# Kernel optimization log

Hardware: AMD Instinct MI355X
Metric: run time of the kernel (lower is better)

Reference implementation:

```python
import jax, jax.numpy as jnp
import numpy as np

B, L1, CTX_TXT, C, NH, HD = 2, 4096, 512, 2048, 16, 128
IMG_LEN = 257           # hard-coded image-context length in WanI2VCrossAttentionProcessor
L2 = IMG_LEN + CTX_TXT
EPS = 1e-6


def setup_inputs() -> dict:
    key = jax.random.key(0)
    ks = jax.random.split(key, 16)
    s = 0.02
    w = lambda k: jax.random.normal(k, (C, C), jnp.float32) * s
    bvec = lambda k: jax.random.normal(k, (C,), jnp.float32) * s
    return {
        "x": jax.random.normal(ks[0], (B, L1, C), jnp.float32),
        "context": jax.random.normal(ks[1], (B, L2, C), jnp.float32),
        "context_lens": jax.random.randint(ks[2], (B,), 1, CTX_TXT + 1, jnp.int32),
        "Wq": w(ks[3]), "bq": bvec(ks[4]), "gq": jnp.ones((C,), jnp.float32),
        "Wk": w(ks[5]), "bk": bvec(ks[6]), "gk": jnp.ones((C,), jnp.float32),
        "Wv": w(ks[7]), "bv": bvec(ks[8]),
        "Wki": w(ks[9]), "bki": bvec(ks[10]), "gki": jnp.ones((C,), jnp.float32),
        "Wvi": w(ks[11]), "bvi": bvec(ks[12]),
        "Wo": w(ks[13]), "bo": bvec(ks[14]),
    }


def rms_norm(x, g):
    # RMSNorm over full channel dim (applied before head reshape, as in source)
    return x * jax.lax.rsqrt(jnp.mean(x * x, axis=-1, keepdims=True) + EPS) * g


def attention(q, k, v, key_mask=None):
    # q: [b, Lq, n, d]; k, v: [b, Lk, n, d]
    scale = 1.0 / np.sqrt(HD).astype(np.float32)
    scores = jnp.einsum('bqnd,bknd->bnqk', q, k) * scale
    if key_mask is not None:
        scores = jnp.where(key_mask, scores, jnp.finfo(scores.dtype).min)
    probs = jax.nn.softmax(scores, axis=-1)
    return jnp.einsum('bnqk,bknd->bqnd', probs, v)


def reference(x, context, context_lens, Wq, bq, gq, Wk, bk, gk, Wv, bv,
              Wki, bki, gki, Wvi, bvi, Wo, bo):
    b = x.shape[0]
    ctx_img = context[:, :IMG_LEN]
    ctx_txt = context[:, IMG_LEN:]

    q = rms_norm(x @ Wq + bq, gq).reshape(b, -1, NH, HD)
    k = rms_norm(ctx_txt @ Wk + bk, gk).reshape(b, -1, NH, HD)
    v = (ctx_txt @ Wv + bv).reshape(b, -1, NH, HD)
    k_img = rms_norm(ctx_img @ Wki + bki, gki).reshape(b, -1, NH, HD)
    v_img = (ctx_img @ Wvi + bvi).reshape(b, -1, NH, HD)

    img_x = attention(q, k_img, v_img)  # no k_lens on image branch
    key_mask = (jnp.arange(CTX_TXT)[None, :] < context_lens[:, None])[:, None, None, :]
    txt_x = attention(q, k, v, key_mask)

    out = (txt_x + img_x).reshape(b, -1, NH * HD)
    return out @ Wo + bo
```

## Files before the change

kernel.cpp:

```cpp
#include <hip/hip_runtime.h>

typedef unsigned short u16;
typedef short short8 __attribute__((ext_vector_type(8)));
typedef float f32x4 __attribute__((ext_vector_type(4)));
typedef unsigned short u16x4 __attribute__((ext_vector_type(4)));

__device__ __forceinline__ u16 f2bf(float f) {
  unsigned u = __builtin_bit_cast(unsigned, f);
  u += 0x7fffu + ((u >> 16) & 1u);
  return (u16)(u >> 16);
}
__device__ __forceinline__ float bf2f(u16 s) {
  unsigned u = ((unsigned)s) << 16;
  return __builtin_bit_cast(float, u);
}
__device__ __forceinline__ unsigned cvtpk_bf16(float a, float b) {
  unsigned r;
  asm("v_cvt_pk_bf16_f32 %0, %1, %2" : "=v"(r) : "v"(a), "v"(b));
  return r;
}

#if __has_builtin(__builtin_amdgcn_exp2f)
#define EXP2F(x) __builtin_amdgcn_exp2f(x)
#else
#define EXP2F(x) exp2f(x)
#endif

#define MFMA32(a, b, c) __builtin_amdgcn_mfma_f32_16x16x32_bf16(a, b, c, 0, 0, 0)

#define GLDS16(gp, lp)                                                         \
  __builtin_amdgcn_global_load_lds(                                            \
      (__attribute__((address_space(1))) void*)(gp),                           \
      (__attribute__((address_space(3))) void*)(lp), 16, 0, 0)

__global__ __launch_bounds__(256) void cast_bf16_k(const float* __restrict__ in,
                                                   u16* __restrict__ out, int n4) {
  int i = blockIdx.x * 256 + threadIdx.x;
  if (i >= n4) return;
  float4 v = ((const float4*)in)[i];
  u16x4 o = { f2bf(v.x), f2bf(v.y), f2bf(v.z), f2bf(v.w) };
  ((u16x4*)out)[i] = o;
}

__global__ __launch_bounds__(256) void transw_k(const float* W0, const float* W1,
                                                const float* W2, const float* W3,
                                                const float* W4, const float* W5,
                                                u16* __restrict__ Wt) {
  int z = blockIdx.z;
  const float* W = z == 0 ? W0 : z == 1 ? W1 : z == 2 ? W2 : z == 3 ? W3 : z == 4 ? W4 : W5;
  u16* T = Wt + (size_t)z * 2048 * 2048;
  __shared__ float tile[64][65];
  int k0 = blockIdx.x * 64, n0 = blockIdx.y * 64;
  int c4 = (threadIdx.x & 15) * 4;
  int r = threadIdx.x >> 4;
#pragma unroll
  for (int i = 0; i < 4; ++i) {
    int row = r + i * 16;
    float4 v = *(const float4*)(W + (size_t)(k0 + row) * 2048 + n0 + c4);
    tile[row][c4 + 0] = v.x; tile[row][c4 + 1] = v.y;
    tile[row][c4 + 2] = v.z; tile[row][c4 + 3] = v.w;
  }
  __syncthreads();
#pragma unroll
  for (int i = 0; i < 4; ++i) {
    int nrow = r + i * 16;
    u16x4 o = { f2bf(tile[c4 + 0][nrow]), f2bf(tile[c4 + 1][nrow]),
                f2bf(tile[c4 + 2][nrow]), f2bf(tile[c4 + 3][nrow]) };
    *(u16x4*)(T + (size_t)(n0 + nrow) * 2048 + k0 + c4) = o;
  }
}

struct GemmJob {
  const u16* A; const u16* Bt; const float* bias; void* out;
  int M; int mode; int ldo;
};
struct GemmJobs { GemmJob j[8]; };

__global__ __launch_bounds__(256) void gemm_k(GemmJobs jobs) {
  GemmJob J = jobs.j[blockIdx.z];
  const int m0 = blockIdx.x * 128;
  if (m0 >= J.M) return;
  const int n0 = blockIdx.y * 128;
  __shared__ u16 Asm[2][128 * 32];
  __shared__ u16 Bsm[2][128 * 32];
  const int tid = threadIdx.x;
  const int lane = tid & 63;
  const int l15 = lane & 15, quad = lane >> 4;
  const int wave = tid >> 6;
  const int wr = (wave >> 1) * 64, wc = (wave & 1) * 64;
  f32x4 acc[4][4] = {};
  const int g0 = tid, g1 = tid + 256;
  const u16* ag0 = J.A + (size_t)(m0 + (g0 >> 2)) * 2048 + (g0 & 3) * 8;
  const u16* ag1 = J.A + (size_t)(m0 + (g1 >> 2)) * 2048 + (g1 & 3) * 8;
  const u16* bg0 = J.Bt + (size_t)(n0 + (g0 >> 2)) * 2048 + (g0 & 3) * 8;
  const u16* bg1 = J.Bt + (size_t)(n0 + (g1 >> 2)) * 2048 + (g1 & 3) * 8;

  auto stage = [&](int buf, int k0) {
    GLDS16(ag0 + k0, &Asm[buf][g0 * 8]);
    GLDS16(ag1 + k0, &Asm[buf][g1 * 8]);
    GLDS16(bg0 + k0, &Bsm[buf][g0 * 8]);
    GLDS16(bg1 + k0, &Bsm[buf][g1 * 8]);
  };
  stage(0, 0);
  for (int k0 = 0; k0 < 2048; k0 += 32) {
    const int cb = (k0 >> 5) & 1;
    __syncthreads();
    if (k0 + 32 < 2048) stage(cb ^ 1, k0 + 32);
    short8 af[4], bf[4];
#pragma unroll
    for (int mi = 0; mi < 4; ++mi)
      af[mi] = *(const short8*)(&Asm[cb][(wr + mi * 16 + l15) * 32 + quad * 8]);
#pragma unroll
    for (int ni = 0; ni < 4; ++ni)
      bf[ni] = *(const short8*)(&Bsm[cb][(wc + ni * 16 + l15) * 32 + quad * 8]);
    __builtin_amdgcn_s_setprio(1);
#pragma unroll
    for (int mi = 0; mi < 4; ++mi)
#pragma unroll
      for (int ni = 0; ni < 4; ++ni)
        acc[mi][ni] = __builtin_amdgcn_mfma_f32_16x16x32_bf16(af[mi], bf[ni], acc[mi][ni], 0, 0, 0);
    __builtin_amdgcn_s_setprio(0);
  }
#pragma unroll
  for (int mi = 0; mi < 4; ++mi) {
#pragma unroll
    for (int ni = 0; ni < 4; ++ni) {
      int nn = n0 + wc + ni * 16 + l15;
      float bv = J.bias[nn];
#pragma unroll
      for (int r = 0; r < 4; ++r) {
        int mm = m0 + wr + mi * 16 + quad * 4 + r;
        if (mm >= J.M) continue;
        float v = acc[mi][ni][r] + bv;
        if (J.mode == 0) {
          ((u16*)J.out)[(size_t)mm * J.ldo + nn] = f2bf(v);
        } else if (J.mode == 1) {
          int ml = mm & 31;
          int mp = (mm & ~31) | (((ml >> 2) & 3) * 8 + (ml >> 4) * 4 + (ml & 3));
          ((u16*)J.out)[(size_t)nn * J.ldo + mp] = f2bf(v);
        } else {
          ((float*)J.out)[(size_t)mm * J.ldo + nn] = v;
        }
      }
    }
  }
}

__global__ __launch_bounds__(512, 2) void gemm256_k(const u16* __restrict__ A,
                                                    const u16* __restrict__ Bt,
                                                    const float* __restrict__ bias,
                                                    void* __restrict__ out,
                                                    int mode) {
  const int m0 = blockIdx.x * 256, n0 = blockIdx.y * 256;
  __shared__ u16 lds[3][2][256 * 32];
  const int tid = threadIdx.x, lane = tid & 63;
  const int l15 = lane & 15, quad = lane >> 4;
  const int wave = tid >> 6;
  const int wr = wave >> 2;
  const int wc = wave & 3;
  const int srow = tid >> 2;
  const int sc = ((tid & 3) ^ ((srow >> 1) & 3)) * 8;
  const u16* Ag = A + (size_t)(m0 + srow) * 2048 + sc;
  const u16* Bg = Bt + (size_t)(n0 + srow) * 2048 + sc;
  const int lxor = (l15 >> 1) & 3;
  f32x4 acc[8][4] = {};

  auto stage = [&](int buf, int kt) {
    const size_t ko = (size_t)kt * 32;
    u16* dA = &lds[buf][0][tid * 8];
    u16* dB = &lds[buf][1][tid * 8];
    GLDS16(Ag + ko, dA);
    GLDS16(Ag + (size_t)128 * 2048 + ko, dA + 4096);
    GLDS16(Bg + ko, dB);
    GLDS16(Bg + (size_t)128 * 2048 + ko, dB + 4096);
  };

  stage(0, 0);
  stage(1, 1);
  int cb = 0;
  for (int t = 0; t < 64; ++t) {
    if (t < 63) asm volatile("s_waitcnt vmcnt(4)" ::: "memory");
    else        asm volatile("s_waitcnt vmcnt(0)" ::: "memory");
    __builtin_amdgcn_s_barrier();
    if (t + 2 < 64) stage((cb == 0) ? 2 : cb - 1, t + 2);
    const u16* Ab = &lds[cb][0][(size_t)wr * 128 * 32];
    const u16* Bb = &lds[cb][1][0];
    short8 bfr[4];
#pragma unroll
    for (int ni = 0; ni < 4; ++ni) {
      const int rn = wc * 64 + ni * 16 + l15;
      bfr[ni] = *(const short8*)(Bb + rn * 32 + ((quad ^ lxor) * 8));
    }
#pragma unroll
    for (int mi = 0; mi < 8; ++mi) {
      const int rm = mi * 16 + l15;
      short8 a = *(const short8*)(Ab + rm * 32 + ((quad ^ lxor) * 8));
      __builtin_amdgcn_s_setprio(1);
#pragma unroll
      for (int ni = 0; ni < 4; ++ni)
        acc[mi][ni] = MFMA32(a, bfr[ni], acc[mi][ni]);
      __builtin_amdgcn_s_setprio(0);
    }
    cb = (cb == 2) ? 0 : cb + 1;
  }
#pragma unroll
  for (int mi = 0; mi < 8; ++mi) {
#pragma unroll
    for (int ni = 0; ni < 4; ++ni) {
      const int nn = n0 + wc * 64 + ni * 16 + l15;
      const float bv = bias[nn];
      const int mm = m0 + wr * 128 + mi * 16 + quad * 4;
      if (mode == 0) {
        u16* op = (u16*)out + (size_t)mm * 2048 + nn;
#pragma unroll
        for (int r = 0; r < 4; ++r) op[(size_t)r * 2048] = f2bf(acc[mi][ni][r] + bv);
      } else {
        float* op = (float*)out + (size_t)mm * 2048 + nn;
#pragma unroll
        for (int r = 0; r < 4; ++r) op[(size_t)r * 2048] = acc[mi][ni][r] + bv;
      }
    }
  }
}

__global__ __launch_bounds__(256) void rmsnorm_k(u16* __restrict__ buf,
                                                 const float* __restrict__ g) {
  const int row = blockIdx.x, tid = threadIdx.x;
  u16* p = buf + (size_t)row * 2048 + tid * 8;
  short8 v = *(short8*)p;
  float x[8]; float s = 0.f;
#pragma unroll
  for (int i = 0; i < 8; ++i) { x[i] = bf2f((u16)v[i]); s += x[i] * x[i]; }
#pragma unroll
  for (int o = 1; o < 64; o <<= 1) s += __shfl_xor(s, o, 64);
  __shared__ float ws4[4];
  if ((tid & 63) == 0) ws4[tid >> 6] = s;
  __syncthreads();
  float tot = ws4[0] + ws4[1] + ws4[2] + ws4[3];
  float scale = rsqrtf(tot * (1.0f / 2048.0f) + 1e-6f);
  const float* gp = g + tid * 8;
  short8 o8;
#pragma unroll
  for (int i = 0; i < 8; ++i) o8[i] = (short)f2bf(x[i] * scale * gp[i]);
  *(short8*)p = o8;
}

__global__ __launch_bounds__(512) void attn_k(const u16* __restrict__ Q,
                                              const u16* __restrict__ Kt,
                                              const u16* __restrict__ Vt,
                                              const u16* __restrict__ Ki,
                                              const u16* __restrict__ Vi,
                                              const int* __restrict__ lens,
                                              u16* __restrict__ out) {
  const int lid = blockIdx.x + 16 * (blockIdx.y + 16 * blockIdx.z);
  const int w = (lid & 7) * 64 + (lid >> 3);
  const int qx = w & 15, hb = w >> 4;
  const int h = hb & 15, b = hb >> 4;

  const int tid = threadIdx.x, lane = tid & 63, wave = tid >> 6;
  const int l15 = lane & 15, quad = lane >> 4;
  const int qbase = qx * 256 + wave * 32;
  const float scale2 = 0.12752358514837517f;
  const float NEGINF = -__builtin_inff();
  __shared__ u16 Ksm[2][2][32 * 128];
  __shared__ u16 Vsm[2][2][128 * 32];

  short8 qf[2][4];
#pragma unroll
  for (int h2 = 0; h2 < 2; ++h2) {
    const u16* qb = Q + ((size_t)(b * 4096 + qbase + h2 * 16 + l15)) * 2048 + h * 128 + quad * 8;
#pragma unroll
    for (int kc = 0; kc < 4; ++kc) qf[h2][kc] = *(const short8*)(qb + kc * 32);
  }

  const int krow = tid >> 4;
  const int kcc = ((tid & 15) ^ (krow & 7)) * 8;
  const int vd = tid >> 2;
  const int vcs = ((tid & 3) ^ ((vd >> 1) & 3)) * 8;
  const int kxor = l15 & 7;
  const int vxor = (l15 >> 1) & 3;

  f32x4 accv[2][8];
  u16x4 oimg[2][8];
  float run_m[2], run_l[2];

  auto phase = [&](const u16* Kb, const u16* Vb, int Lv, int LK) {
    run_m[0] = run_m[1] = NEGINF;
    run_l[0] = run_l[1] = 0.f;
#pragma unroll
    for (int h2 = 0; h2 < 2; ++h2)
#pragma unroll
      for (int dt = 0; dt < 8; ++dt)
#pragma unroll
        for (int r = 0; r < 4; ++r) accv[h2][dt][r] = 0.f;
    const u16* kg = Kb + (size_t)krow * 2048 + kcc;
    const u16* vg = Vb + (size_t)vd * LK + vcs;
    const int ntiles = (Lv + 63) >> 6;
    auto stage = [&](int buf, int t) {
      const int kvA = t * 64;
      const int sA = (kvA < LK - 32) ? kvA : (LK - 32);
      const int sB = (kvA + 32 < LK - 32) ? (kvA + 32) : (LK - 32);
      GLDS16(kg + (size_t)sA * 2048, &Ksm[buf][0][tid * 8]);
      GLDS16(kg + (size_t)sB * 2048, &Ksm[buf][1][tid * 8]);
      GLDS16(vg + sA, &Vsm[buf][0][tid * 8]);
      GLDS16(vg + sB, &Vsm[buf][1][tid * 8]);
    };
    stage(0, 0);
    __syncthreads();
    for (int t = 0; t < ntiles; ++t) {
      const int cb = t & 1;
      if (t + 1 < ntiles) stage(cb ^ 1, t + 1);

      f32x4 s[2][4];
#pragma unroll
      for (int h2 = 0; h2 < 2; ++h2)
#pragma unroll
        for (int kb = 0; kb < 4; ++kb)
#pragma unroll
          for (int r = 0; r < 4; ++r) s[h2][kb][r] = 0.f;
      {
        short8 kA[2][4];
#pragma unroll
        for (int kc = 0; kc < 4; ++kc) {
          const int c0 = ((kc * 4 + quad) ^ kxor) * 8;
          kA[0][kc] = *(const short8*)(&Ksm[cb][0][l15 * 128 + c0]);
          kA[1][kc] = *(const short8*)(&Ksm[cb][0][(16 + l15) * 128 + c0]);
        }
        __builtin_amdgcn_s_setprio(1);
#pragma unroll
        for (int h2 = 0; h2 < 2; ++h2)
#pragma unroll
          for (int kc = 0; kc < 4; ++kc) {
            s[h2][0] = MFMA32(kA[0][kc], qf[h2][kc], s[h2][0]);
            s[h2][1] = MFMA32(kA[1][kc], qf[h2][kc], s[h2][1]);
          }
        __builtin_amdgcn_s_setprio(0);
      }
      {
        short8 kB[2][4];
#pragma unroll
        for (int kc = 0; kc < 4; ++kc) {
          const int c0 = ((kc * 4 + quad) ^ kxor) * 8;
          kB[0][kc] = *(const short8*)(&Ksm[cb][1][l15 * 128 + c0]);
          kB[1][kc] = *(const short8*)(&Ksm[cb][1][(16 + l15) * 128 + c0]);
        }
        __builtin_amdgcn_s_setprio(1);
#pragma unroll
        for (int h2 = 0; h2 < 2; ++h2)
#pragma unroll
          for (int kc = 0; kc < 4; ++kc) {
            s[h2][2] = MFMA32(kB[0][kc], qf[h2][kc], s[h2][2]);
            s[h2][3] = MFMA32(kB[1][kc], qf[h2][kc], s[h2][3]);
          }
        __builtin_amdgcn_s_setprio(0);
      }

      const int kvA = t * 64;
      if (kvA + 64 > Lv) {
#pragma unroll
        for (int h2 = 0; h2 < 2; ++h2)
#pragma unroll
          for (int kb = 0; kb < 4; ++kb)
#pragma unroll
            for (int r = 0; r < 4; ++r) {
              const int ki = kvA + kb * 16 + quad * 4 + r;
              if (ki >= Lv) s[h2][kb][r] = NEGINF;
            }
      }

      float al[2];
      short8 pfA[2], pfB[2];
#pragma unroll
      for (int h2 = 0; h2 < 2; ++h2) {
        float m0 = fmaxf(fmaxf(s[h2][0][0], s[h2][0][1]), fmaxf(s[h2][0][2], s[h2][0][3]));
        float m1 = fmaxf(fmaxf(s[h2][1][0], s[h2][1][1]), fmaxf(s[h2][1][2], s[h2][1][3]));
        float m2 = fmaxf(fmaxf(s[h2][2][0], s[h2][2][1]), fmaxf(s[h2][2][2], s[h2][2][3]));
        float m3 = fmaxf(fmaxf(s[h2][3][0], s[h2][3][1]), fmaxf(s[h2][3][2], s[h2][3][3]));
        float mx = fmaxf(fmaxf(m0, m1), fmaxf(m2, m3));
        mx = fmaxf(mx, __shfl_xor(mx, 16, 64));
        mx = fmaxf(mx, __shfl_xor(mx, 32, 64));
        const float nm = (mx - run_m[h2] > 62.0f) ? mx : run_m[h2];
        al[h2] = EXP2F((run_m[h2] - nm) * scale2);
        run_m[h2] = nm;
        const float nmc = -nm * scale2;
        float p[4][4], psum = 0.f;
#pragma unroll
        for (int kb = 0; kb < 4; ++kb)
#pragma unroll
          for (int r = 0; r < 4; ++r) {
            p[kb][r] = EXP2F(__builtin_fmaf(s[h2][kb][r], scale2, nmc));
            psum += p[kb][r];
          }
        run_l[h2] = __builtin_fmaf(run_l[h2], al[h2], psum);
        union { short8 s8; unsigned u[4]; } pa, pb;
        pa.u[0] = cvtpk_bf16(p[0][0], p[0][1]);
        pa.u[1] = cvtpk_bf16(p[0][2], p[0][3]);
        pa.u[2] = cvtpk_bf16(p[1][0], p[1][1]);
        pa.u[3] = cvtpk_bf16(p[1][2], p[1][3]);
        pb.u[0] = cvtpk_bf16(p[2][0], p[2][1]);
        pb.u[1] = cvtpk_bf16(p[2][2], p[2][3]);
        pb.u[2] = cvtpk_bf16(p[3][0], p[3][1]);
        pb.u[3] = cvtpk_bf16(p[3][2], p[3][3]);
        pfA[h2] = pa.s8;
        pfB[h2] = pb.s8;
      }
      if (t != 0 && __ballot((al[0] < 1.0f) || (al[1] < 1.0f))) {
#pragma unroll
        for (int h2 = 0; h2 < 2; ++h2)
#pragma unroll
          for (int dt = 0; dt < 8; ++dt)
#pragma unroll
            for (int r = 0; r < 4; ++r) accv[h2][dt][r] *= al[h2];
      }

      __builtin_amdgcn_s_setprio(1);
#pragma unroll
      for (int dt = 0; dt < 8; ++dt) {
        const int vo = (dt * 16 + l15) * 32 + ((quad ^ vxor) * 8);
        short8 vfA = *(const short8*)(&Vsm[cb][0][vo]);
        short8 vfB = *(const short8*)(&Vsm[cb][1][vo]);
        accv[0][dt] = MFMA32(vfA, pfA[0], accv[0][dt]);
        accv[1][dt] = MFMA32(vfA, pfA[1], accv[1][dt]);
        accv[0][dt] = MFMA32(vfB, pfB[0], accv[0][dt]);
        accv[1][dt] = MFMA32(vfB, pfB[1], accv[1][dt]);
      }
      __builtin_amdgcn_s_setprio(0);
      __syncthreads();
    }
  };

  const u16* Kb_i = Ki + (size_t)(b * 288) * 2048 + h * 128;
  const u16* Vb_i = Vi + ((size_t)(b * 16 + h) * 128) * 288;
  phase(Kb_i, Vb_i, 257, 288);
#pragma unroll
  for (int h2 = 0; h2 < 2; ++h2) {
    float a = run_l[h2] + __shfl_xor(run_l[h2], 16, 64);
    float lt = a + __shfl_xor(a, 32, 64);
    float inv = 1.0f / lt;
#pragma unroll
    for (int dt = 0; dt < 8; ++dt) {
      u16x4 w2 = { f2bf(accv[h2][dt][0] * inv), f2bf(accv[h2][dt][1] * inv),
                   f2bf(accv[h2][dt][2] * inv), f2bf(accv[h2][dt][3] * inv) };
      oimg[h2][dt] = w2;
    }
  }
  const u16* Kb_t = Kt + (size_t)(b * 512) * 2048 + h * 128;
  const u16* Vb_t = Vt + ((size_t)(b * 16 + h) * 128) * 512;
  phase(Kb_t, Vb_t, lens[b], 512);
#pragma unroll
  for (int h2 = 0; h2 < 2; ++h2) {
    float a = run_l[h2] + __shfl_xor(run_l[h2], 16, 64);
    float lt = a + __shfl_xor(a, 32, 64);
    float inv = 1.0f / lt;
    u16* ob = out + ((size_t)(b * 4096 + qbase + h2 * 16 + l15)) * 2048 + h * 128 + quad * 4;
#pragma unroll
    for (int dt = 0; dt < 8; ++dt) {
      u16x4 w2 = { f2bf(bf2f(oimg[h2][dt][0]) + accv[h2][dt][0] * inv),
                   f2bf(bf2f(oimg[h2][dt][1]) + accv[h2][dt][1] * inv),
                   f2bf(bf2f(oimg[h2][dt][2]) + accv[h2][dt][2] * inv),
                   f2bf(bf2f(oimg[h2][dt][3]) + accv[h2][dt][3] * inv) };
      *(u16x4*)(ob + dt * 16) = w2;
    }
  }
}

extern "C" void kernel_launch(void* const* d_in, const int* in_sizes, int n_in,
                              void* d_out, int out_size, void* d_ws, size_t ws_size,
                              hipStream_t stream) {
  const float* x   = (const float*)d_in[0];
  const float* ctx = (const float*)d_in[1];
  const int* lens  = (const int*)d_in[2];
  const float* Wq  = (const float*)d_in[3];
  const float* bq  = (const float*)d_in[4];
  const float* gq  = (const float*)d_in[5];
  const float* Wk  = (const float*)d_in[6];
  const float* bk  = (const float*)d_in[7];
  const float* gk  = (const float*)d_in[8];
  const float* Wv  = (const float*)d_in[9];
  const float* bv  = (const float*)d_in[10];
  const float* Wki = (const float*)d_in[11];
  const float* bki = (const float*)d_in[12];
  const float* gki = (const float*)d_in[13];
  const float* Wvi = (const float*)d_in[14];
  const float* bvi = (const float*)d_in[15];
  const float* Wo  = (const float*)d_in[16];
  const float* bo  = (const float*)d_in[17];
  float* out = (float*)d_out;

  char* p = (char*)d_ws;
  u16* x_bf   = (u16*)p; p += (size_t)8192 * 2048 * 2;
  u16* ctx_bf = (u16*)p; p += (size_t)2 * 769 * 2048 * 2;
  u16* Wt     = (u16*)p; p += (size_t)6 * 2048 * 2048 * 2;
  u16* Qb     = (u16*)p; p += (size_t)8192 * 2048 * 2;
  u16* Ktxt   = (u16*)p; p += (size_t)2 * 512 * 2048 * 2;
  u16* Vtt    = (u16*)p; p += (size_t)2 * 16 * 128 * 512 * 2;
  u16* Kimg   = (u16*)p; p += (size_t)2 * 288 * 2048 * 2;
  u16* Vti    = (u16*)p; p += (size_t)2 * 16 * 128 * 288 * 2;
  u16* attn_o = x_bf;

  cast_bf16_k<<<16384, 256, 0, stream>>>(x, x_bf, 8192 * 2048 / 4);
  cast_bf16_k<<<3076, 256, 0, stream>>>(ctx, ctx_bf, 2 * 769 * 2048 / 4);
  transw_k<<<dim3(32, 32, 6), 256, 0, stream>>>(Wq, Wk, Wv, Wki, Wvi, Wo, Wt);

  gemm256_k<<<dim3(32, 8), 512, 0, stream>>>(x_bf, Wt + 0ull * 4194304, bq, Qb, 0);

  GemmJobs jc = {};
  for (int b = 0; b < 2; ++b) {
    const u16* txtA = ctx_bf + (size_t)(b * 769 + 257) * 2048;
    const u16* imgA = ctx_bf + (size_t)(b * 769) * 2048;
    jc.j[0 + b] = { txtA, Wt + 1ull * 4194304, bk,  Ktxt + (size_t)b * 512 * 2048, 512, 0, 2048 };
    jc.j[2 + b] = { txtA, Wt + 2ull * 4194304, bv,  Vtt  + (size_t)b * 2048 * 512, 512, 1, 512 };
    jc.j[4 + b] = { imgA, Wt + 3ull * 4194304, bki, Kimg + (size_t)b * 288 * 2048, 257, 0, 2048 };
    jc.j[6 + b] = { imgA, Wt + 4ull * 4194304, bvi, Vti  + (size_t)b * 2048 * 288, 257, 1, 288 };
  }
  gemm_k<<<dim3(4, 16, 8), 256, 0, stream>>>(jc);

  rmsnorm_k<<<8192, 256, 0, stream>>>(Qb, gq);
  rmsnorm_k<<<1024, 256, 0, stream>>>(Ktxt, gk);
  rmsnorm_k<<<576, 256, 0, stream>>>(Kimg, gki);

  attn_k<<<dim3(16, 16, 2), 512, 0, stream>>>(Qb, Ktxt, Vtt, Kimg, Vti, lens, attn_o);

  gemm256_k<<<dim3(32, 8), 512, 0, stream>>>(attn_o, Wt + 5ull * 4194304, bo, out, 1);
}
```

Measured before the change: 514.2 us.

## Use BK=64 double-buffered GEMM tiles and remap attention blocks per XCD

The 256x256 GEMM now stages 64-wide K slices with a double buffer instead of 32-wide slices with a triple buffer. This halves the number of barriers and loop iterations, and an XOR swizzle over 8 chunks keeps LDS reads conflict-free. The trade-off is that the explicit vmcnt-based prefetch depth is replaced by a plain __syncthreads, so load latency is hidden less. The attention kernel also changes its block-to-(head,batch,qtile) mapping so each XCD handles two heads across both batches, which is meant to improve L2 reuse of K/V.

```diff
diff --git a/kernel.cpp b/kernel.cpp
--- a/kernel.cpp
+++ b/kernel.cpp
@@ -152,56 +152,55 @@
                                                     void* __restrict__ out,
                                                     int mode) {
   const int m0 = blockIdx.x * 256, n0 = blockIdx.y * 256;
-  __shared__ u16 lds[3][2][256 * 32];
+  __shared__ u16 lds[2][2][256 * 64];
   const int tid = threadIdx.x, lane = tid & 63;
   const int l15 = lane & 15, quad = lane >> 4;
   const int wave = tid >> 6;
   const int wr = wave >> 2;
   const int wc = wave & 3;
-  const int srow = tid >> 2;
-  const int sc = ((tid & 3) ^ ((srow >> 1) & 3)) * 8;
-  const u16* Ag = A + (size_t)(m0 + srow) * 2048 + sc;
-  const u16* Bg = Bt + (size_t)(n0 + srow) * 2048 + sc;
-  const int lxor = (l15 >> 1) & 3;
   f32x4 acc[8][4] = {};
 
   auto stage = [&](int buf, int kt) {
-    const size_t ko = (size_t)kt * 32;
-    u16* dA = &lds[buf][0][tid * 8];
-    u16* dB = &lds[buf][1][tid * 8];
-    GLDS16(Ag + ko, dA);
-    GLDS16(Ag + (size_t)128 * 2048 + ko, dA + 4096);
-    GLDS16(Bg + ko, dB);
-    GLDS16(Bg + (size_t)128 * 2048 + ko, dB + 4096);
+    const int ko = kt * 64;
+#pragma unroll
+    for (int j = 0; j < 4; ++j) {
+      const int c = tid + 512 * j;
+      const int row = c >> 3;
+      const int scc = (((c & 7) ^ (row & 7)) * 8);
+      GLDS16(A + (size_t)(m0 + row) * 2048 + ko + scc, &lds[buf][0][(size_t)c * 8]);
+      GLDS16(Bt + (size_t)(n0 + row) * 2048 + ko + scc, &lds[buf][1][(size_t)c * 8]);
+    }
   };
 
   stage(0, 0);
-  stage(1, 1);
-  int cb = 0;
-  for (int t = 0; t < 64; ++t) {
-    if (t < 63) asm volatile("s_waitcnt vmcnt(4)" ::: "memory");
-    else        asm volatile("s_waitcnt vmcnt(0)" ::: "memory");
-    __builtin_amdgcn_s_barrier();
-    if (t + 2 < 64) stage((cb == 0) ? 2 : cb - 1, t + 2);
-    const u16* Ab = &lds[cb][0][(size_t)wr * 128 * 32];
+  for (int t = 0; t < 32; ++t) {
+    const int cb = t & 1;
+    __syncthreads();
+    if (t + 1 < 32) stage(cb ^ 1, t + 1);
+    const u16* Ab = &lds[cb][0][0];
     const u16* Bb = &lds[cb][1][0];
-    short8 bfr[4];
-#pragma unroll
-    for (int ni = 0; ni < 4; ++ni) {
-      const int rn = wc * 64 + ni * 16 + l15;
-      bfr[ni] = *(const short8*)(Bb + rn * 32 + ((quad ^ lxor) * 8));
-    }
+    short8 bfr[2][4];
+#pragma unroll
+    for (int kk = 0; kk < 2; ++kk)
+#pragma unroll
+      for (int ni = 0; ni < 4; ++ni) {
+        const int rn = wc * 64 + ni * 16 + l15;
+        bfr[kk][ni] = *(const short8*)(Bb + rn * 64 + (((kk * 4 + quad) ^ (rn & 7)) * 8));
+      }
 #pragma unroll
     for (int mi = 0; mi < 8; ++mi) {
-      const int rm = mi * 16 + l15;
-      short8 a = *(const short8*)(Ab + rm * 32 + ((quad ^ lxor) * 8));
+      const int rm = wr * 128 + mi * 16 + l15;
+      short8 a0 = *(const short8*)(Ab + rm * 64 + (((0 + quad) ^ (rm & 7)) * 8));
+      short8 a1 = *(const short8*)(Ab + rm * 64 + (((4 + quad) ^ (rm & 7)) * 8));
       __builtin_amdgcn_s_setprio(1);
 #pragma unroll
       for (int ni = 0; ni < 4; ++ni)
-        acc[mi][ni] = MFMA32(a, bfr[ni], acc[mi][ni]);
+        acc[mi][ni] = MFMA32(a0, bfr[0][ni], acc[mi][ni]);
+#pragma unroll
+      for (int ni = 0; ni < 4; ++ni)
+        acc[mi][ni] = MFMA32(a1, bfr[1][ni], acc[mi][ni]);
       __builtin_amdgcn_s_setprio(0);
     }
-    cb = (cb == 2) ? 0 : cb + 1;
   }
 #pragma unroll
   for (int mi = 0; mi < 8; ++mi) {
@@ -253,9 +252,10 @@
                                               const int* __restrict__ lens,
                                               u16* __restrict__ out) {
   const int lid = blockIdx.x + 16 * (blockIdx.y + 16 * blockIdx.z);
-  const int w = (lid & 7) * 64 + (lid >> 3);
-  const int qx = w & 15, hb = w >> 4;
-  const int h = hb & 15, b = hb >> 4;
+  const int xcd = lid & 7, i = lid >> 3;
+  const int h = xcd * 2 + (i & 1);
+  const int b = (i >> 1) & 1;
+  const int qx = i >> 2;
 
   const int tid = threadIdx.x, lane = tid & 63, wave = tid >> 6;
   const int l15 = lane & 15, quad = lane >> 4;
```

After: 502.9 us. 1.02x faster.
